# Kernel tuning notes

Hardware: AMD Instinct MI355X
Metric: run time of the kernel (lower is better)

The kernel has to match this reference:

```python
import jax, jax.numpy as jnp
import numpy as np

B, C, H, W = 8, 256, 64, 64
IC = 64  # inter_channels


def conv1x1(x, w, b):
    # x: [B,C,H,W], w: [O,C], b: [O]
    return jnp.einsum('bchw,oc->bohw', x, w) + b[None, :, None, None]


def maxpool2(x):
    # 2x2 max pool, stride 2. x: [B,C,H,W]
    b, c, h, w = x.shape
    return x.reshape(b, c, h // 2, 2, w // 2, 2).max(axis=(3, 5))


def setup_inputs() -> dict:
    key = jax.random.key(0)
    ks = jax.random.split(key, 9)
    s_in = 1.0 / np.sqrt(C)
    s_ic = 1.0 / np.sqrt(IC)
    return {
        'x': jax.random.normal(ks[0], (B, C, H, W), dtype=jnp.float32),
        'g_w': jax.random.uniform(ks[1], (IC, C), jnp.float32, -s_in, s_in),
        'g_b': jax.random.uniform(ks[2], (IC,), jnp.float32, -s_in, s_in),
        'theta_w': jax.random.uniform(ks[3], (IC, C), jnp.float32, -s_in, s_in),
        'theta_b': jax.random.uniform(ks[4], (IC,), jnp.float32, -s_in, s_in),
        'phi_w': jax.random.uniform(ks[5], (IC, C), jnp.float32, -s_in, s_in),
        'phi_b': jax.random.uniform(ks[6], (IC,), jnp.float32, -s_in, s_in),
        'W_w': jax.random.uniform(ks[7], (C, IC), jnp.float32, -np.sqrt(6.0 / IC), np.sqrt(6.0 / IC)),
        'W_b': jax.random.uniform(ks[8], (C,), jnp.float32, -s_ic, s_ic),
    }


def reference(x, g_w, g_b, theta_w, theta_b, phi_w, phi_b, W_w, W_b):
    b, c, h, w = x.shape
    n = h * w                     # query positions
    m = (h // 2) * (w // 2)       # pooled key/value positions

    v = maxpool2(conv1x1(x, g_w, g_b)).reshape(b, IC, m).transpose(0, 2, 1)   # [b,m,ic]
    q = conv1x1(x, theta_w, theta_b).reshape(b, IC, n).transpose(0, 2, 1)     # [b,n,ic]
    k = maxpool2(conv1x1(x, phi_w, phi_b)).reshape(b, IC, m)                  # [b,ic,m]

    attn = jax.nn.softmax(jnp.einsum('bni,bim->bnm', q, k), axis=-1)          # [b,n,m]
    attended = jnp.einsum('bnm,bmi->bni', attn, v)                            # [b,n,ic]
    attended = attended.transpose(0, 2, 1).reshape(b, IC, h, w)
    # F.interpolate to (h,w) is identity here: attended already has spatial (h,w)
    return conv1x1(attended, W_w, W_b) + x
```

## Files before the change

kernel.cpp:

```cpp
#include <hip/hip_runtime.h>

typedef unsigned short ushort_t;
typedef unsigned int   uint_t;

typedef __attribute__((ext_vector_type(8))) short  short8;
typedef __attribute__((ext_vector_type(4))) short  short4v;
typedef __attribute__((ext_vector_type(4))) float  float4v;

#define BB    8
#define CC    256
#define HH    64
#define WW2   64
#define NPIX  4096
#define MPOS  1024
#define ICH   64

__device__ __forceinline__ float bf2f(ushort_t u) {
  return __uint_as_float(((uint_t)u) << 16);
}
__device__ __forceinline__ ushort_t f2bf(float f) {
  uint_t i = __float_as_uint(f);
  uint_t r = (i + 0x7FFFu + ((i >> 16) & 1u)) >> 16;
  return (ushort_t)r;
}
__device__ __forceinline__ ushort_t f2bf_rna(float f) {
  return (ushort_t)((__float_as_uint(f) + 0x8000u) >> 16);
}
__device__ __forceinline__ uint_t pack2(float a, float b) {
  return (uint_t)f2bf(a) | ((uint_t)f2bf(b) << 16);
}

__global__ __launch_bounds__(256) void prep_kernel(
    const float* __restrict__ theta_w, const float* __restrict__ phi_w,
    const float* __restrict__ g_w, const float* __restrict__ W_w,
    const float* __restrict__ theta_b, const float* __restrict__ phi_b,
    const float* __restrict__ g_b,
    ushort_t* __restrict__ wA2, ushort_t* __restrict__ Wbf2,
    float* __restrict__ biasAll) {
  int i = blockIdx.x * 256 + threadIdx.x;
  if (i < 49152) {
    float v = (i < 16384) ? theta_w[i]
            : (i < 32768) ? phi_w[i - 16384]
                          : g_w[i - 32768];
    int o = i >> 8, c = i & 255;
    wA2[(c >> 3) * 1536 + o * 8 + (c & 7)] = f2bf(v);
  } else if (i < 65536) {
    int j = i - 49152;
    int o = j >> 6, ic = j & 63;
    Wbf2[(ic >> 3) * 2048 + o * 8 + (ic & 7)] = f2bf(W_w[j]);
  } else if (i < 65600)    biasAll[i - 65536] = theta_b[i - 65536];
  else if (i < 65664)      biasAll[i - 65536] = phi_b[i - 65600];
  else if (i < 65728)      biasAll[i - 65536] = g_b[i - 65664];
}

__global__ __launch_bounds__(256, 2) void qkv_kernel(
    const float* __restrict__ x, const ushort_t* __restrict__ wA2,
    const float* __restrict__ biasAll,
    ushort_t* __restrict__ qbuf, ushort_t* __restrict__ kTbuf,
    ushort_t* __restrict__ vTbuf) {
  __shared__ __align__(16) ushort_t Bsu[64 * 256];
  uint4* Bs16 = (uint4*)Bsu;
  int tid = threadIdx.x;
  int wave = tid >> 6, lane = tid & 63;
  int quad = lane >> 4, col = lane & 15;
  int b = blockIdx.x >> 6, t = blockIdx.x & 63;
  int rj = t >> 1, h = t & 1;

  {
    int pos = tid & 63, cg = tid >> 6;
    int prow = pos >> 5, pcol = pos & 31;
    const float* xsrc = x + (size_t)b * (CC * NPIX) +
                        (size_t)(2 * rj + prow) * WW2 + h * 32 + pcol;
#pragma unroll
    for (int g = 0; g < 8; ++g) {
      float v[8];
#pragma unroll
      for (int j = 0; j < 8; ++j)
        v[j] = xsrc[(size_t)(cg * 64 + g * 8 + j) * NPIX];
      uint4 w;
      w.x = pack2(v[0], v[1]);
      w.y = pack2(v[2], v[3]);
      w.z = pack2(v[4], v[5]);
      w.w = pack2(v[6], v[7]);
      int jb = cg * 8 + g;
      Bs16[pos * 32 + (jb & ~7) + ((jb & 7) ^ (pos & 7))] = w;
    }
  }
  __syncthreads();

  float4v acc[3][4];
#pragma unroll
  for (int ot = 0; ot < 3; ++ot) {
    int ob = wave * 48 + ot * 16 + quad * 4;
    float4v bv;
#pragma unroll
    for (int r = 0; r < 4; ++r) bv[r] = biasAll[ob + r];
#pragma unroll
    for (int s = 0; s < 4; ++s) acc[ot][s] = bv;
  }

  const uint4* wA16 = (const uint4*)wA2;
#pragma unroll
  for (int ks = 0; ks < 8; ++ks) {
    int kblk = ks * 4 + quad;
    short8 aw[3];
#pragma unroll
    for (int ot = 0; ot < 3; ++ot) {
      uint4 a = wA16[kblk * 192 + wave * 48 + ot * 16 + col];
      aw[ot] = *(const short8*)&a;
    }
#pragma unroll
    for (int s = 0; s < 4; ++s) {
      int lp = s * 16 + col;
      uint4 braw = Bs16[lp * 32 + (kblk & ~7) + ((kblk & 7) ^ (lp & 7))];
      short8 bx = *(const short8*)&braw;
#pragma unroll
      for (int ot = 0; ot < 3; ++ot)
        acc[ot][s] = __builtin_amdgcn_mfma_f32_16x16x32_bf16(aw[ot], bx, acc[ot][s], 0, 0, 0);
    }
  }

#pragma unroll
  for (int ot = 0; ot < 3; ++ot) {
    int ob = wave * 48 + ot * 16;
    if (ob < 64) {
#pragma unroll
      for (int s = 0; s < 4; ++s) {
        int n = (2 * rj + (s >> 1)) * WW2 + h * 32 + (s & 1) * 16 + col;
        uint2 u;
        u.x = pack2(acc[ot][s][0], acc[ot][s][1]);
        u.y = pack2(acc[ot][s][2], acc[ot][s][3]);
        *(uint2*)&qbuf[((size_t)(b * NPIX + n)) * ICH + ob + quad * 4] = u;
      }
    } else if (ob < 128) {
#pragma unroll
      for (int s = 0; s < 2; ++s) {
        float4v pm;
#pragma unroll
        for (int r = 0; r < 4; ++r) {
          float v = fmaxf(acc[ot][s][r], acc[ot][s + 2][r]);
          pm[r] = fmaxf(v, __shfl_xor(v, 1));
        }
        if ((lane & 1) == 0) {
          int m = rj * 32 + h * 16 + s * 8 + (col >> 1);
          uint2 u;
          u.x = pack2(pm[0], pm[1]);
          u.y = pack2(pm[2], pm[3]);
          *(uint2*)&kTbuf[((size_t)(b * MPOS + m)) * ICH + (ob - 64) + quad * 4] = u;
        }
      }
    } else {
#pragma unroll
      for (int s = 0; s < 2; ++s) {
        float4v pm;
#pragma unroll
        for (int r = 0; r < 4; ++r) {
          float v = fmaxf(acc[ot][s][r], acc[ot][s + 2][r]);
          pm[r] = fmaxf(v, __shfl_xor(v, 1));
        }
        if ((lane & 1) == 0) {
          int m = rj * 32 + h * 16 + s * 8 + (col >> 1);
#pragma unroll
          for (int r = 0; r < 4; ++r)
            vTbuf[((size_t)(b * ICH + (ob - 128) + quad * 4 + r)) * MPOS + m] = f2bf(pm[r]);
        }
      }
    }
  }
}

__global__ __launch_bounds__(256, 2) void attn_out_kernel(
    const ushort_t* __restrict__ qbuf, const ushort_t* __restrict__ kTbuf,
    const ushort_t* __restrict__ vTbuf, const ushort_t* __restrict__ Wbf2,
    const float* __restrict__ W_b, const float* __restrict__ x,
    float* __restrict__ out) {
  __shared__ __align__(16) ushort_t Ks[2][64 * 64];
  __shared__ __align__(16) ushort_t Vs[2][64 * 64];
  __shared__ __align__(16) ushort_t Ps[64 * 72];
  int tid  = threadIdx.x;
  int wave = tid >> 6, lane = tid & 63;
  int quad = lane >> 4, col = lane & 15;
  int b = blockIdx.x >> 6, qt = blockIdx.x & 63;

  const ushort_t* qrow = qbuf + ((size_t)(b * NPIX + qt * 64 + wave * 16 + col)) * ICH;
  short8 aQ0 = *(const short8*)&qrow[quad * 8];
  short8 aQ1 = *(const short8*)&qrow[32 + quad * 8];

  int krow0 = tid >> 3,           kblk0 = tid & 7;
  int krow1 = (tid + 256) >> 3,   kblk1 = tid & 7;
  int vic = tid >> 2, vseg = tid & 3;

  const uint4* ksrc0 = (const uint4*)(kTbuf + ((size_t)(b * MPOS)) * ICH);
  const ushort_t* vbase = vTbuf + ((size_t)(b * ICH + vic)) * MPOS;

  {
    uint4 k0 = ksrc0[tid], k1 = ksrc0[tid + 256];
    const uint4* vsrc = (const uint4*)(vbase + vseg * 16);
    uint4 v0 = vsrc[0], v1 = vsrc[1];
    *(uint4*)&Ks[0][krow0 * 64 + ((kblk0 ^ (krow0 & 7)) * 8)] = k0;
    *(uint4*)&Ks[0][krow1 * 64 + ((kblk1 ^ (krow1 & 7)) * 8)] = k1;
    *(uint4*)&Vs[0][vic * 64 + (((vseg * 2 + 0) ^ (vic & 7)) * 8)] = v0;
    *(uint4*)&Vs[0][vic * 64 + (((vseg * 2 + 1) ^ (vic & 7)) * 8)] = v1;
  }
  __syncthreads();

  const float4v zero4 = {0.f, 0.f, 0.f, 0.f};
  float l_lane[4] = {0.f, 0.f, 0.f, 0.f};
  float4v o_acc[4];
#pragma unroll
  for (int t = 0; t < 4; ++t) o_acc[t] = zero4;

  for (int kt = 0; kt < 16; ++kt) {
    uint4 nk0, nk1, nv0, nv1;
    if (kt < 15) {
      const uint4* ksrc = (const uint4*)(kTbuf + ((size_t)(b * MPOS + (kt + 1) * 64)) * ICH);
      nk0 = ksrc[tid];
      nk1 = ksrc[tid + 256];
      const uint4* vsrc = (const uint4*)(vbase + (kt + 1) * 64 + vseg * 16);
      nv0 = vsrc[0];
      nv1 = vsrc[1];
    }
    int buf = kt & 1;

    float4v s_acc[4];
#pragma unroll
    for (int t = 0; t < 4; ++t) {
      float4v s = zero4;
      short8 bk0 = *(const short8*)&Ks[buf][(t * 16 + col) * 64 + ((quad ^ (col & 7)) * 8)];
      s = __builtin_amdgcn_mfma_f32_16x16x32_bf16(aQ0, bk0, s, 0, 0, 0);
      short8 bk1 = *(const short8*)&Ks[buf][(t * 16 + col) * 64 + (((4 + quad) ^ (col & 7)) * 8)];
      s = __builtin_amdgcn_mfma_f32_16x16x32_bf16(aQ1, bk1, s, 0, 0, 0);
      s_acc[t] = s;
    }

#pragma unroll
    for (int r = 0; r < 4; ++r) {
      int prow = (wave * 16 + quad * 4 + r) * 72;
#pragma unroll
      for (int t = 0; t < 4; ++t) {
        float pv = __expf(s_acc[t][r]);
        l_lane[r] += pv;
        Ps[prow + t * 16 + col] = f2bf_rna(pv);
      }
    }

#pragma unroll
    for (int kk = 0; kk < 2; ++kk) {
      short8 ap = *(const short8*)&Ps[(wave * 16 + col) * 72 + kk * 32 + quad * 8];
#pragma unroll
      for (int t = 0; t < 4; ++t) {
        short8 bv = *(const short8*)&Vs[buf][(t * 16 + col) * 64 + (((kk * 4 + quad) ^ (col & 7)) * 8)];
        o_acc[t] = __builtin_amdgcn_mfma_f32_16x16x32_bf16(ap, bv, o_acc[t], 0, 0, 0);
      }
    }

    if (kt < 15) {
      int nbuf = buf ^ 1;
      *(uint4*)&Ks[nbuf][krow0 * 64 + ((kblk0 ^ (krow0 & 7)) * 8)] = nk0;
      *(uint4*)&Ks[nbuf][krow1 * 64 + ((kblk1 ^ (krow1 & 7)) * 8)] = nk1;
      *(uint4*)&Vs[nbuf][vic * 64 + (((vseg * 2 + 0) ^ (vic & 7)) * 8)] = nv0;
      *(uint4*)&Vs[nbuf][vic * 64 + (((vseg * 2 + 1) ^ (vic & 7)) * 8)] = nv1;
      __syncthreads();
    }
  }

#pragma unroll
  for (int r = 0; r < 4; ++r) {
    float l = l_lane[r];
    l += __shfl_xor(l, 1);
    l += __shfl_xor(l, 2);
    l += __shfl_xor(l, 4);
    l += __shfl_xor(l, 8);
    float inv = 1.0f / l;
    int prow = (wave * 16 + quad * 4 + r) * 72;
#pragma unroll
    for (int t = 0; t < 4; ++t)
      Ps[prow + t * 16 + col] = f2bf(o_acc[t][r] * inv);
  }

  float4v cacc[16];
#pragma unroll
  for (int ot = 0; ot < 16; ++ot) {
    float bv = W_b[ot * 16 + col];
    float4v bvec = {bv, bv, bv, bv};
    cacc[ot] = bvec;
  }
  const uint4* W16 = (const uint4*)Wbf2;
#pragma unroll
  for (int ks = 0; ks < 2; ++ks) {
    short8 ap = *(const short8*)&Ps[(wave * 16 + col) * 72 + ks * 32 + quad * 8];
#pragma unroll
    for (int ot = 0; ot < 16; ++ot) {
      uint4 wr = W16[(ks * 4 + quad) * 256 + ot * 16 + col];
      short8 wf = *(const short8*)&wr;
      cacc[ot] = __builtin_amdgcn_mfma_f32_16x16x32_bf16(ap, wf, cacc[ot], 0, 0, 0);
    }
  }

  int pbase = qt * 64 + wave * 16 + quad * 4;
#pragma unroll
  for (int ot = 0; ot < 16; ++ot) {
    int o = ot * 16 + col;
    size_t idx = ((size_t)(b * CC + o)) * NPIX + pbase;
    float4 xv = *(const float4*)&x[idx];
    float4 ov;
    ov.x = cacc[ot][0] + xv.x;
    ov.y = cacc[ot][1] + xv.y;
    ov.z = cacc[ot][2] + xv.z;
    ov.w = cacc[ot][3] + xv.w;
    *(float4*)&out[idx] = ov;
  }
}

extern "C" void kernel_launch(void* const* d_in, const int* in_sizes, int n_in,
                              void* d_out, int out_size, void* d_ws, size_t ws_size,
                              hipStream_t stream) {
  const float* x       = (const float*)d_in[0];
  const float* g_w     = (const float*)d_in[1];
  const float* g_b     = (const float*)d_in[2];
  const float* theta_w = (const float*)d_in[3];
  const float* theta_b = (const float*)d_in[4];
  const float* phi_w   = (const float*)d_in[5];
  const float* phi_b   = (const float*)d_in[6];
  const float* W_w     = (const float*)d_in[7];
  const float* W_b     = (const float*)d_in[8];
  (void)in_sizes; (void)n_in; (void)out_size; (void)ws_size;

  char* ws = (char*)d_ws;
  ushort_t* wA2     = (ushort_t*)(ws + 0);
  ushort_t* Wbf2    = (ushort_t*)(ws + 98304);
  float*    biasAll = (float*)(ws + 131072);
  ushort_t* qbuf    = (ushort_t*)(ws + 262144);
  ushort_t* kTbuf   = (ushort_t*)(ws + 4456448);
  ushort_t* vTbuf   = (ushort_t*)(ws + 5505024);
  float* out = (float*)d_out;

  prep_kernel<<<257, 256, 0, stream>>>(theta_w, phi_w, g_w, W_w,
                                       theta_b, phi_b, g_b,
                                       wA2, Wbf2, biasAll);
  qkv_kernel<<<512, 256, 0, stream>>>(x, wA2, biasAll, qbuf, kTbuf, vTbuf);
  attn_out_kernel<<<512, 256, 0, stream>>>(qbuf, kTbuf, vTbuf, Wbf2, W_b, x, out);
}
```

Baseline: 132.2 us.

## Split key range across wave halves in attention and halve qkv tile

The attention kernel now uses 512 threads. Two groups of four waves each take half of the key/value tiles for the same 64 queries. Their softmax denominators are combined through shared memory, and each half then computes half of the output channels from both partial P@V results. The x residual load is hoisted before the output GEMM, and s_setprio is raised around the MFMA sections. The qkv kernel uses smaller 32-position tiles over twice as many blocks with higher occupancy bounds. The goal is more parallelism and latency hiding, at the cost of losing K/V double buffering and adding extra barriers.

```diff
diff --git a/kernel.cpp b/kernel.cpp
--- a/kernel.cpp
+++ b/kernel.cpp
@@ -53,50 +53,50 @@
   else if (i < 65728)      biasAll[i - 65536] = g_b[i - 65664];
 }
 
-__global__ __launch_bounds__(256, 2) void qkv_kernel(
+__global__ __launch_bounds__(256, 4) void qkv_kernel(
     const float* __restrict__ x, const ushort_t* __restrict__ wA2,
     const float* __restrict__ biasAll,
     ushort_t* __restrict__ qbuf, ushort_t* __restrict__ kTbuf,
     ushort_t* __restrict__ vTbuf) {
-  __shared__ __align__(16) ushort_t Bsu[64 * 256];
+  __shared__ __align__(16) ushort_t Bsu[32 * 256];
   uint4* Bs16 = (uint4*)Bsu;
   int tid = threadIdx.x;
   int wave = tid >> 6, lane = tid & 63;
   int quad = lane >> 4, col = lane & 15;
-  int b = blockIdx.x >> 6, t = blockIdx.x & 63;
-  int rj = t >> 1, h = t & 1;
+  int b = blockIdx.x >> 7, t = blockIdx.x & 127;
+  int rj = t >> 2, cq = t & 3;
 
   {
-    int pos = tid & 63, cg = tid >> 6;
-    int prow = pos >> 5, pcol = pos & 31;
+    int pos = tid & 31, cg = tid >> 5;
+    int prow = pos >> 4, pcol = pos & 15;
     const float* xsrc = x + (size_t)b * (CC * NPIX) +
-                        (size_t)(2 * rj + prow) * WW2 + h * 32 + pcol;
-#pragma unroll
-    for (int g = 0; g < 8; ++g) {
+                        (size_t)(2 * rj + prow) * WW2 + cq * 16 + pcol;
+#pragma unroll
+    for (int g = 0; g < 4; ++g) {
       float v[8];
 #pragma unroll
       for (int j = 0; j < 8; ++j)
-        v[j] = xsrc[(size_t)(cg * 64 + g * 8 + j) * NPIX];
+        v[j] = xsrc[(size_t)(cg * 32 + g * 8 + j) * NPIX];
       uint4 w;
       w.x = pack2(v[0], v[1]);
       w.y = pack2(v[2], v[3]);
       w.z = pack2(v[4], v[5]);
       w.w = pack2(v[6], v[7]);
-      int jb = cg * 8 + g;
+      int jb = cg * 4 + g;
       Bs16[pos * 32 + (jb & ~7) + ((jb & 7) ^ (pos & 7))] = w;
     }
   }
   __syncthreads();
 
-  float4v acc[3][4];
+  float4v acc[3][2];
 #pragma unroll
   for (int ot = 0; ot < 3; ++ot) {
     int ob = wave * 48 + ot * 16 + quad * 4;
     float4v bv;
 #pragma unroll
     for (int r = 0; r < 4; ++r) bv[r] = biasAll[ob + r];
-#pragma unroll
-    for (int s = 0; s < 4; ++s) acc[ot][s] = bv;
+    acc[ot][0] = bv;
+    acc[ot][1] = bv;
   }
 
   const uint4* wA16 = (const uint4*)wA2;
@@ -110,7 +110,7 @@
       aw[ot] = *(const short8*)&a;
     }
 #pragma unroll
-    for (int s = 0; s < 4; ++s) {
+    for (int s = 0; s < 2; ++s) {
       int lp = s * 16 + col;
       uint4 braw = Bs16[lp * 32 + (kblk & ~7) + ((kblk & 7) ^ (lp & 7))];
       short8 bx = *(const short8*)&braw;
@@ -125,82 +125,81 @@
     int ob = wave * 48 + ot * 16;
     if (ob < 64) {
 #pragma unroll
-      for (int s = 0; s < 4; ++s) {
-        int n = (2 * rj + (s >> 1)) * WW2 + h * 32 + (s & 1) * 16 + col;
+      for (int s = 0; s < 2; ++s) {
+        int n = (2 * rj + s) * WW2 + cq * 16 + col;
         uint2 u;
         u.x = pack2(acc[ot][s][0], acc[ot][s][1]);
         u.y = pack2(acc[ot][s][2], acc[ot][s][3]);
         *(uint2*)&qbuf[((size_t)(b * NPIX + n)) * ICH + ob + quad * 4] = u;
       }
     } else if (ob < 128) {
-#pragma unroll
-      for (int s = 0; s < 2; ++s) {
-        float4v pm;
-#pragma unroll
-        for (int r = 0; r < 4; ++r) {
-          float v = fmaxf(acc[ot][s][r], acc[ot][s + 2][r]);
-          pm[r] = fmaxf(v, __shfl_xor(v, 1));
-        }
-        if ((lane & 1) == 0) {
-          int m = rj * 32 + h * 16 + s * 8 + (col >> 1);
-          uint2 u;
-          u.x = pack2(pm[0], pm[1]);
-          u.y = pack2(pm[2], pm[3]);
-          *(uint2*)&kTbuf[((size_t)(b * MPOS + m)) * ICH + (ob - 64) + quad * 4] = u;
-        }
+      float4v pm;
+#pragma unroll
+      for (int r = 0; r < 4; ++r) {
+        float v = fmaxf(acc[ot][0][r], acc[ot][1][r]);
+        pm[r] = fmaxf(v, __shfl_xor(v, 1));
+      }
+      if ((lane & 1) == 0) {
+        int m = rj * 32 + cq * 8 + (col >> 1);
+        uint2 u;
+        u.x = pack2(pm[0], pm[1]);
+        u.y = pack2(pm[2], pm[3]);
+        *(uint2*)&kTbuf[((size_t)(b * MPOS + m)) * ICH + (ob - 64) + quad * 4] = u;
       }
     } else {
-#pragma unroll
-      for (int s = 0; s < 2; ++s) {
-        float4v pm;
-#pragma unroll
-        for (int r = 0; r < 4; ++r) {
-          float v = fmaxf(acc[ot][s][r], acc[ot][s + 2][r]);
-          pm[r] = fmaxf(v, __shfl_xor(v, 1));
-        }
-        if ((lane & 1) == 0) {
-          int m = rj * 32 + h * 16 + s * 8 + (col >> 1);
-#pragma unroll
-          for (int r = 0; r < 4; ++r)
-            vTbuf[((size_t)(b * ICH + (ob - 128) + quad * 4 + r)) * MPOS + m] = f2bf(pm[r]);
-        }
-      }
-    }
-  }
-}
-
-__global__ __launch_bounds__(256, 2) void attn_out_kernel(
+      float4v pm;
+#pragma unroll
+      for (int r = 0; r < 4; ++r) {
+        float v = fmaxf(acc[ot][0][r], acc[ot][1][r]);
+        pm[r] = fmaxf(v, __shfl_xor(v, 1));
+      }
+      if ((lane & 1) == 0) {
+        int m = rj * 32 + cq * 8 + (col >> 1);
+#pragma unroll
+        for (int r = 0; r < 4; ++r)
+          vTbuf[((size_t)(b * ICH + (ob - 128) + quad * 4 + r)) * MPOS + m] = f2bf(pm[r]);
+      }
+    }
+  }
+}
+
+__global__ __launch_bounds__(512, 2) void attn_out_kernel(
     const ushort_t* __restrict__ qbuf, const ushort_t* __restrict__ kTbuf,
     const ushort_t* __restrict__ vTbuf, const ushort_t* __restrict__ Wbf2,
     const float* __restrict__ W_b, const float* __restrict__ x,
     float* __restrict__ out) {
-  __shared__ __align__(16) ushort_t Ks[2][64 * 64];
-  __shared__ __align__(16) ushort_t Vs[2][64 * 64];
-  __shared__ __align__(16) ushort_t Ps[64 * 72];
+  __shared__ __align__(16) ushort_t SH[25600];
   int tid  = threadIdx.x;
-  int wave = tid >> 6, lane = tid & 63;
+  int wid  = tid >> 6, lane = tid & 63;
   int quad = lane >> 4, col = lane & 15;
+  int wrow = wid & 3, whalf = wid >> 2;
   int b = blockIdx.x >> 6, qt = blockIdx.x & 63;
-
-  const ushort_t* qrow = qbuf + ((size_t)(b * NPIX + qt * 64 + wave * 16 + col)) * ICH;
+  int hid = tid & 255;
+
+  ushort_t* Ksh = SH + whalf * 4096;
+  ushort_t* Vsh = SH + 8192 + whalf * 4096;
+  ushort_t* Psh = SH + 16384 + whalf * 4608;
+
+  const ushort_t* qrow = qbuf + ((size_t)(b * NPIX + qt * 64 + wrow * 16 + col)) * ICH;
   short8 aQ0 = *(const short8*)&qrow[quad * 8];
   short8 aQ1 = *(const short8*)&qrow[32 + quad * 8];
 
-  int krow0 = tid >> 3,           kblk0 = tid & 7;
-  int krow1 = (tid + 256) >> 3,   kblk1 = tid & 7;
-  int vic = tid >> 2, vseg = tid & 3;
-
-  const uint4* ksrc0 = (const uint4*)(kTbuf + ((size_t)(b * MPOS)) * ICH);
+  int krow0 = hid >> 3,         kblk0 = hid & 7;
+  int krow1 = (hid + 256) >> 3, kblk1 = hid & 7;
+  int vic = hid >> 2, vseg = hid & 3;
+  int ktbase = whalf * 8;
+
+  const uint4* ksrc = (const uint4*)(kTbuf + (size_t)b * MPOS * ICH);
   const ushort_t* vbase = vTbuf + ((size_t)(b * ICH + vic)) * MPOS;
 
   {
-    uint4 k0 = ksrc0[tid], k1 = ksrc0[tid + 256];
-    const uint4* vsrc = (const uint4*)(vbase + vseg * 16);
+    uint4 k0 = ksrc[ktbase * 512 + hid], k1 = ksrc[ktbase * 512 + 256 + hid];
+    const uint4* vsrc = (const uint4*)(vbase + ktbase * 64 + vseg * 16);
     uint4 v0 = vsrc[0], v1 = vsrc[1];
-    *(uint4*)&Ks[0][krow0 * 64 + ((kblk0 ^ (krow0 & 7)) * 8)] = k0;
-    *(uint4*)&Ks[0][krow1 * 64 + ((kblk1 ^ (krow1 & 7)) * 8)] = k1;
-    *(uint4*)&Vs[0][vic * 64 + (((vseg * 2 + 0) ^ (vic & 7)) * 8)] = v0;
-    *(uint4*)&Vs[0][vic * 64 + (((vseg * 2 + 1) ^ (vic & 7)) * 8)] = v1;
+    *(uint4*)&Ksh[krow0 * 64 + ((kblk0 ^ (krow0 & 7)) * 8)] = k0;
+    *(uint4*)&Ksh[krow1 * 64 + ((kblk1 ^ (krow1 & 7)) * 8)] = k1;
+    *(uint4*)&Vsh[vic * 64 + (((vseg * 2 + 0) ^ (vic & 7)) * 8)] = v0;
+    *(uint4*)&Vsh[vic * 64 + (((vseg * 2 + 1) ^ (vic & 7)) * 8)] = v1;
   }
   __syncthreads();
 
@@ -210,104 +209,130 @@
 #pragma unroll
   for (int t = 0; t < 4; ++t) o_acc[t] = zero4;
 
-  for (int kt = 0; kt < 16; ++kt) {
+  for (int i = 0; i < 8; ++i) {
     uint4 nk0, nk1, nv0, nv1;
-    if (kt < 15) {
-      const uint4* ksrc = (const uint4*)(kTbuf + ((size_t)(b * MPOS + (kt + 1) * 64)) * ICH);
-      nk0 = ksrc[tid];
-      nk1 = ksrc[tid + 256];
-      const uint4* vsrc = (const uint4*)(vbase + (kt + 1) * 64 + vseg * 16);
+    if (i < 7) {
+      int kt = ktbase + i + 1;
+      nk0 = ksrc[kt * 512 + hid];
+      nk1 = ksrc[kt * 512 + 256 + hid];
+      const uint4* vsrc = (const uint4*)(vbase + kt * 64 + vseg * 16);
       nv0 = vsrc[0];
       nv1 = vsrc[1];
     }
-    int buf = kt & 1;
 
     float4v s_acc[4];
+    __builtin_amdgcn_s_setprio(1);
 #pragma unroll
     for (int t = 0; t < 4; ++t) {
       float4v s = zero4;
-      short8 bk0 = *(const short8*)&Ks[buf][(t * 16 + col) * 64 + ((quad ^ (col & 7)) * 8)];
+      short8 bk0 = *(const short8*)&Ksh[(t * 16 + col) * 64 + ((quad ^ (col & 7)) * 8)];
       s = __builtin_amdgcn_mfma_f32_16x16x32_bf16(aQ0, bk0, s, 0, 0, 0);
-      short8 bk1 = *(const short8*)&Ks[buf][(t * 16 + col) * 64 + (((4 + quad) ^ (col & 7)) * 8)];
+      short8 bk1 = *(const short8*)&Ksh[(t * 16 + col) * 64 + (((4 + quad) ^ (col & 7)) * 8)];
       s = __builtin_amdgcn_mfma_f32_16x16x32_bf16(aQ1, bk1, s, 0, 0, 0);
       s_acc[t] = s;
     }
+    __builtin_amdgcn_s_setprio(0);
 
 #pragma unroll
     for (int r = 0; r < 4; ++r) {
-      int prow = (wave * 16 + quad * 4 + r) * 72;
+      int prow = (wrow * 16 + quad * 4 + r) * 72;
 #pragma unroll
       for (int t = 0; t < 4; ++t) {
         float pv = __expf(s_acc[t][r]);
         l_lane[r] += pv;
-        Ps[prow + t * 16 + col] = f2bf_rna(pv);
-      }
-    }
-
+        Psh[prow + t * 16 + col] = f2bf_rna(pv);
+      }
+    }
+
+    __builtin_amdgcn_s_setprio(1);
 #pragma unroll
     for (int kk = 0; kk < 2; ++kk) {
-      short8 ap = *(const short8*)&Ps[(wave * 16 + col) * 72 + kk * 32 + quad * 8];
+      short8 ap = *(const short8*)&Psh[(wrow * 16 + col) * 72 + kk * 32 + quad * 8];
 #pragma unroll
       for (int t = 0; t < 4; ++t) {
-        short8 bv = *(const short8*)&Vs[buf][(t * 16 + col) * 64 + (((kk * 4 + quad) ^ (col & 7)) * 8)];
+        short8 bv = *(const short8*)&Vsh[(t * 16 + col) * 64 + (((kk * 4 + quad) ^ (col & 7)) * 8)];
         o_acc[t] = __builtin_amdgcn_mfma_f32_16x16x32_bf16(ap, bv, o_acc[t], 0, 0, 0);
       }
     }
-
-    if (kt < 15) {
-      int nbuf = buf ^ 1;
-      *(uint4*)&Ks[nbuf][krow0 * 64 + ((kblk0 ^ (krow0 & 7)) * 8)] = nk0;
-      *(uint4*)&Ks[nbuf][krow1 * 64 + ((kblk1 ^ (krow1 & 7)) * 8)] = nk1;
-      *(uint4*)&Vs[nbuf][vic * 64 + (((vseg * 2 + 0) ^ (vic & 7)) * 8)] = nv0;
-      *(uint4*)&Vs[nbuf][vic * 64 + (((vseg * 2 + 1) ^ (vic & 7)) * 8)] = nv1;
-      __syncthreads();
-    }
-  }
-
+    __builtin_amdgcn_s_setprio(0);
+
+    __syncthreads();
+    if (i < 7) {
+      *(uint4*)&Ksh[krow0 * 64 + ((kblk0 ^ (krow0 & 7)) * 8)] = nk0;
+      *(uint4*)&Ksh[krow1 * 64 + ((kblk1 ^ (krow1 & 7)) * 8)] = nk1;
+      *(uint4*)&Vsh[vic * 64 + (((vseg * 2 + 0) ^ (vic & 7)) * 8)] = nv0;
+      *(uint4*)&Vsh[vic * 64 + (((vseg * 2 + 1) ^ (vic & 7)) * 8)] = nv1;
+    }
+    __syncthreads();
+  }
+
+  float* lbuf = (float*)SH;
+#pragma unroll
+  for (int r = 0; r < 4; ++r) lbuf[tid * 4 + r] = l_lane[r];
+  __syncthreads();
+  float inv_l[4];
 #pragma unroll
   for (int r = 0; r < 4; ++r) {
-    float l = l_lane[r];
+    float l = l_lane[r] + lbuf[(tid ^ 256) * 4 + r];
     l += __shfl_xor(l, 1);
     l += __shfl_xor(l, 2);
     l += __shfl_xor(l, 4);
     l += __shfl_xor(l, 8);
-    float inv = 1.0f / l;
-    int prow = (wave * 16 + quad * 4 + r) * 72;
+    inv_l[r] = 1.0f / l;
+  }
+
+#pragma unroll
+  for (int r = 0; r < 4; ++r) {
+    int prow = (wrow * 16 + quad * 4 + r) * 72;
 #pragma unroll
     for (int t = 0; t < 4; ++t)
-      Ps[prow + t * 16 + col] = f2bf(o_acc[t][r] * inv);
-  }
-
-  float4v cacc[16];
-#pragma unroll
-  for (int ot = 0; ot < 16; ++ot) {
-    float bv = W_b[ot * 16 + col];
+      Psh[prow + t * 16 + col] = f2bf(o_acc[t][r] * inv_l[r]);
+  }
+  __syncthreads();
+
+  float4v cacc[8];
+#pragma unroll
+  for (int ot = 0; ot < 8; ++ot) {
+    float bv = W_b[whalf * 128 + ot * 16 + col];
     float4v bvec = {bv, bv, bv, bv};
     cacc[ot] = bvec;
   }
+
+  int pbase = qt * 64 + wrow * 16 + quad * 4;
+  float4 xv[8];
+#pragma unroll
+  for (int ot = 0; ot < 8; ++ot) {
+    int o = whalf * 128 + ot * 16 + col;
+    xv[ot] = *(const float4*)&x[((size_t)(b * CC + o)) * NPIX + pbase];
+  }
+
   const uint4* W16 = (const uint4*)Wbf2;
-#pragma unroll
-  for (int ks = 0; ks < 2; ++ks) {
-    short8 ap = *(const short8*)&Ps[(wave * 16 + col) * 72 + ks * 32 + quad * 8];
-#pragma unroll
-    for (int ot = 0; ot < 16; ++ot) {
-      uint4 wr = W16[(ks * 4 + quad) * 256 + ot * 16 + col];
-      short8 wf = *(const short8*)&wr;
-      cacc[ot] = __builtin_amdgcn_mfma_f32_16x16x32_bf16(ap, wf, cacc[ot], 0, 0, 0);
-    }
-  }
-
-  int pbase = qt * 64 + wave * 16 + quad * 4;
-#pragma unroll
-  for (int ot = 0; ot < 16; ++ot) {
-    int o = ot * 16 + col;
+  __builtin_amdgcn_s_setprio(1);
+#pragma unroll
+  for (int h = 0; h < 2; ++h) {
+    const ushort_t* Ph = SH + 16384 + h * 4608;
+#pragma unroll
+    for (int ks = 0; ks < 2; ++ks) {
+      short8 ap = *(const short8*)&Ph[(wrow * 16 + col) * 72 + ks * 32 + quad * 8];
+#pragma unroll
+      for (int ot = 0; ot < 8; ++ot) {
+        uint4 wr = W16[(ks * 4 + quad) * 256 + whalf * 128 + ot * 16 + col];
+        short8 wf = *(const short8*)&wr;
+        cacc[ot] = __builtin_amdgcn_mfma_f32_16x16x32_bf16(ap, wf, cacc[ot], 0, 0, 0);
+      }
+    }
+  }
+  __builtin_amdgcn_s_setprio(0);
+
+#pragma unroll
+  for (int ot = 0; ot < 8; ++ot) {
+    int o = whalf * 128 + ot * 16 + col;
     size_t idx = ((size_t)(b * CC + o)) * NPIX + pbase;
-    float4 xv = *(const float4*)&x[idx];
     float4 ov;
-    ov.x = cacc[ot][0] + xv.x;
-    ov.y = cacc[ot][1] + xv.y;
-    ov.z = cacc[ot][2] + xv.z;
-    ov.w = cacc[ot][3] + xv.w;
+    ov.x = cacc[ot][0] + xv[ot].x;
+    ov.y = cacc[ot][1] + xv[ot].y;
+    ov.z = cacc[ot][2] + xv[ot].z;
+    ov.w = cacc[ot][3] + xv[ot].w;
     *(float4*)&out[idx] = ov;
   }
 }
@@ -338,6 +363,6 @@
   prep_kernel<<<257, 256, 0, stream>>>(theta_w, phi_w, g_w, W_w,
                                        theta_b, phi_b, g_b,
                                        wA2, Wbf2, biasAll);
-  qkv_kernel<<<512, 256, 0, stream>>>(x, wA2, biasAll, qbuf, kTbuf, vTbuf);
-  attn_out_kernel<<<512, 256, 0, stream>>>(qbuf, kTbuf, vTbuf, Wbf2, W_b, x, out);
-}
+  qkv_kernel<<<1024, 256, 0, stream>>>(x, wA2, biasAll, qbuf, kTbuf, vTbuf);
+  attn_out_kernel<<<512, 512, 0, stream>>>(qbuf, kTbuf, vTbuf, Wbf2, W_b, x, out);
+}
```

Measured after the change: 137.5 us. +4.0%, slower.

## Load K/V fragments directly from global into registers per wave, drop LDS staging

Applied to the files above, without the earlier changes.

The attention kernel now gives each wave its own independent 16-query job and reads K and V MFMA operands straight from global memory (L2/L1) into registers. K is double-buffered in registers across steps, and LDS is kept only for a per-wave P tile. This removes the block-wide __syncthreads and the LDS store/load traffic for K/V, and adds s_setprio hints around the MFMA sections. The output projection is restructured to compute each output tile and store it immediately, which lowers register pressure. In exchange, each wave reloads the whole K/V for its batch from cache, raising global/L2 traffic fourfold versus block-shared staging. The launch grid must also match the new job mapping in the unseen launcher.

```diff
diff --git a/kernel.cpp b/kernel.cpp
--- a/kernel.cpp
+++ b/kernel.cpp
@@ -174,35 +174,25 @@
     const ushort_t* __restrict__ vTbuf, const ushort_t* __restrict__ Wbf2,
     const float* __restrict__ W_b, const float* __restrict__ x,
     float* __restrict__ out) {
-  __shared__ __align__(16) ushort_t Ks[2][64 * 64];
-  __shared__ __align__(16) ushort_t Vs[2][64 * 64];
-  __shared__ __align__(16) ushort_t Ps[64 * 72];
+  __shared__ __align__(16) ushort_t Ps[4][16 * 72];
   int tid  = threadIdx.x;
-  int wave = tid >> 6, lane = tid & 63;
+  int wid  = tid >> 6, lane = tid & 63;
   int quad = lane >> 4, col = lane & 15;
-  int b = blockIdx.x >> 6, qt = blockIdx.x & 63;
-
-  const ushort_t* qrow = qbuf + ((size_t)(b * NPIX + qt * 64 + wave * 16 + col)) * ICH;
+  int job  = blockIdx.x * 4 + wid;
+  int b    = job >> 8;
+  int qbase = (job & 255) * 16;
+
+  ushort_t* Psw = &Ps[wid][0];
+
+  const ushort_t* kb = kTbuf + (size_t)b * MPOS * ICH;
+  const ushort_t* vb = vTbuf + (size_t)b * ICH * MPOS;
+
+  const ushort_t* qrow = qbuf + ((size_t)(b * NPIX + qbase + col)) * ICH;
   short8 aQ0 = *(const short8*)&qrow[quad * 8];
   short8 aQ1 = *(const short8*)&qrow[32 + quad * 8];
 
-  int krow0 = tid >> 3,           kblk0 = tid & 7;
-  int krow1 = (tid + 256) >> 3,   kblk1 = tid & 7;
-  int vic = tid >> 2, vseg = tid & 3;
-
-  const uint4* ksrc0 = (const uint4*)(kTbuf + ((size_t)(b * MPOS)) * ICH);
-  const ushort_t* vbase = vTbuf + ((size_t)(b * ICH + vic)) * MPOS;
-
-  {
-    uint4 k0 = ksrc0[tid], k1 = ksrc0[tid + 256];
-    const uint4* vsrc = (const uint4*)(vbase + vseg * 16);
-    uint4 v0 = vsrc[0], v1 = vsrc[1];
-    *(uint4*)&Ks[0][krow0 * 64 + ((kblk0 ^ (krow0 & 7)) * 8)] = k0;
-    *(uint4*)&Ks[0][krow1 * 64 + ((kblk1 ^ (krow1 & 7)) * 8)] = k1;
-    *(uint4*)&Vs[0][vic * 64 + (((vseg * 2 + 0) ^ (vic & 7)) * 8)] = v0;
-    *(uint4*)&Vs[0][vic * 64 + (((vseg * 2 + 1) ^ (vic & 7)) * 8)] = v1;
-  }
-  __syncthreads();
+  const ushort_t* kbase = kb + col * ICH + quad * 8;
+  const ushort_t* vbase = vb + (size_t)col * MPOS + quad * 8;
 
   const float4v zero4 = {0.f, 0.f, 0.f, 0.f};
   float l_lane[4] = {0.f, 0.f, 0.f, 0.f};
@@ -210,59 +200,65 @@
 #pragma unroll
   for (int t = 0; t < 4; ++t) o_acc[t] = zero4;
 
-  for (int kt = 0; kt < 16; ++kt) {
-    uint4 nk0, nk1, nv0, nv1;
-    if (kt < 15) {
-      const uint4* ksrc = (const uint4*)(kTbuf + ((size_t)(b * MPOS + (kt + 1) * 64)) * ICH);
-      nk0 = ksrc[tid];
-      nk1 = ksrc[tid + 256];
-      const uint4* vsrc = (const uint4*)(vbase + (kt + 1) * 64 + vseg * 16);
-      nv0 = vsrc[0];
-      nv1 = vsrc[1];
-    }
-    int buf = kt & 1;
-
-    float4v s_acc[4];
-#pragma unroll
-    for (int t = 0; t < 4; ++t) {
-      float4v s = zero4;
-      short8 bk0 = *(const short8*)&Ks[buf][(t * 16 + col) * 64 + ((quad ^ (col & 7)) * 8)];
-      s = __builtin_amdgcn_mfma_f32_16x16x32_bf16(aQ0, bk0, s, 0, 0, 0);
-      short8 bk1 = *(const short8*)&Ks[buf][(t * 16 + col) * 64 + (((4 + quad) ^ (col & 7)) * 8)];
-      s = __builtin_amdgcn_mfma_f32_16x16x32_bf16(aQ1, bk1, s, 0, 0, 0);
-      s_acc[t] = s;
-    }
-
-#pragma unroll
-    for (int r = 0; r < 4; ++r) {
-      int prow = (wave * 16 + quad * 4 + r) * 72;
-#pragma unroll
-      for (int t = 0; t < 4; ++t) {
-        float pv = __expf(s_acc[t][r]);
-        l_lane[r] += pv;
-        Ps[prow + t * 16 + col] = f2bf_rna(pv);
-      }
-    }
-
-#pragma unroll
-    for (int kk = 0; kk < 2; ++kk) {
-      short8 ap = *(const short8*)&Ps[(wave * 16 + col) * 72 + kk * 32 + quad * 8];
-#pragma unroll
-      for (int t = 0; t < 4; ++t) {
-        short8 bv = *(const short8*)&Vs[buf][(t * 16 + col) * 64 + (((kk * 4 + quad) ^ (col & 7)) * 8)];
-        o_acc[t] = __builtin_amdgcn_mfma_f32_16x16x32_bf16(ap, bv, o_acc[t], 0, 0, 0);
-      }
-    }
-
-    if (kt < 15) {
-      int nbuf = buf ^ 1;
-      *(uint4*)&Ks[nbuf][krow0 * 64 + ((kblk0 ^ (krow0 & 7)) * 8)] = nk0;
-      *(uint4*)&Ks[nbuf][krow1 * 64 + ((kblk1 ^ (krow1 & 7)) * 8)] = nk1;
-      *(uint4*)&Vs[nbuf][vic * 64 + (((vseg * 2 + 0) ^ (vic & 7)) * 8)] = nv0;
-      *(uint4*)&Vs[nbuf][vic * 64 + (((vseg * 2 + 1) ^ (vic & 7)) * 8)] = nv1;
-      __syncthreads();
-    }
-  }
+  short8 kfA[8], kfB[8];
+
+#define LOADK(dst, kt)                                                        \
+  _Pragma("unroll")                                                           \
+  for (int t = 0; t < 4; ++t) {                                               \
+    dst[t * 2 + 0] = *(const short8*)&kbase[((kt) * 64 + t * 16) * 64];       \
+    dst[t * 2 + 1] = *(const short8*)&kbase[((kt) * 64 + t * 16) * 64 + 32];  \
+  }
+
+  LOADK(kfA, 0);
+
+#define STEP(kcur, knext, kt)                                                 \
+  {                                                                           \
+    short8 vf[8];                                                             \
+    _Pragma("unroll")                                                         \
+    for (int t = 0; t < 4; ++t) {                                             \
+      _Pragma("unroll")                                                       \
+      for (int kk = 0; kk < 2; ++kk)                                          \
+        vf[t * 2 + kk] =                                                      \
+            *(const short8*)&vbase[t * 16 * MPOS + (kt) * 64 + kk * 32];      \
+    }                                                                         \
+    if ((kt) < 15) { LOADK(knext, (kt) + 1); }                                \
+    float4v s_acc[4];                                                         \
+    __builtin_amdgcn_s_setprio(1);                                            \
+    _Pragma("unroll")                                                         \
+    for (int t = 0; t < 4; ++t) {                                             \
+      float4v s = zero4;                                                      \
+      s = __builtin_amdgcn_mfma_f32_16x16x32_bf16(aQ0, kcur[t * 2 + 0], s, 0, 0, 0); \
+      s = __builtin_amdgcn_mfma_f32_16x16x32_bf16(aQ1, kcur[t * 2 + 1], s, 0, 0, 0); \
+      s_acc[t] = s;                                                           \
+    }                                                                         \
+    __builtin_amdgcn_s_setprio(0);                                            \
+    _Pragma("unroll")                                                         \
+    for (int r = 0; r < 4; ++r) {                                             \
+      int prow = (quad * 4 + r) * 72;                                         \
+      _Pragma("unroll")                                                       \
+      for (int t = 0; t < 4; ++t) {                                           \
+        float pv = __expf(s_acc[t][r]);                                       \
+        l_lane[r] += pv;                                                      \
+        Psw[prow + t * 16 + col] = f2bf_rna(pv);                              \
+      }                                                                       \
+    }                                                                         \
+    __builtin_amdgcn_s_setprio(1);                                            \
+    _Pragma("unroll")                                                         \
+    for (int kk = 0; kk < 2; ++kk) {                                          \
+      short8 ap = *(const short8*)&Psw[col * 72 + kk * 32 + quad * 8];        \
+      _Pragma("unroll")                                                       \
+      for (int t = 0; t < 4; ++t)                                             \
+        o_acc[t] = __builtin_amdgcn_mfma_f32_16x16x32_bf16(ap, vf[t * 2 + kk], o_acc[t], 0, 0, 0); \
+    }                                                                         \
+    __builtin_amdgcn_s_setprio(0);                                            \
+  }
+
+  for (int i = 0; i < 8; ++i) {
+    STEP(kfA, kfB, 2 * i);
+    STEP(kfB, kfA, 2 * i + 1);
+  }
+#undef STEP
+#undef LOADK
 
 #pragma unroll
   for (int r = 0; r < 4; ++r) {
@@ -272,42 +268,31 @@
     l += __shfl_xor(l, 4);
     l += __shfl_xor(l, 8);
     float inv = 1.0f / l;
-    int prow = (wave * 16 + quad * 4 + r) * 72;
+    int prow = (quad * 4 + r) * 72;
 #pragma unroll
     for (int t = 0; t < 4; ++t)
-      Ps[prow + t * 16 + col] = f2bf(o_acc[t][r] * inv);
-  }
-
-  float4v cacc[16];
+      Psw[prow + t * 16 + col] = f2bf(o_acc[t][r] * inv);
+  }
+
+  short8 ap0 = *(const short8*)&Psw[col * 72 + quad * 8];
+  short8 ap1 = *(const short8*)&Psw[col * 72 + 32 + quad * 8];
+  const uint4* W16 = (const uint4*)Wbf2;
+  int pbase = qbase + quad * 4;
 #pragma unroll
   for (int ot = 0; ot < 16; ++ot) {
-    float bv = W_b[ot * 16 + col];
-    float4v bvec = {bv, bv, bv, bv};
-    cacc[ot] = bvec;
-  }
-  const uint4* W16 = (const uint4*)Wbf2;
-#pragma unroll
-  for (int ks = 0; ks < 2; ++ks) {
-    short8 ap = *(const short8*)&Ps[(wave * 16 + col) * 72 + ks * 32 + quad * 8];
-#pragma unroll
-    for (int ot = 0; ot < 16; ++ot) {
-      uint4 wr = W16[(ks * 4 + quad) * 256 + ot * 16 + col];
-      short8 wf = *(const short8*)&wr;
-      cacc[ot] = __builtin_amdgcn_mfma_f32_16x16x32_bf16(ap, wf, cacc[ot], 0, 0, 0);
-    }
-  }
-
-  int pbase = qt * 64 + wave * 16 + quad * 4;
-#pragma unroll
-  for (int ot = 0; ot < 16; ++ot) {
-    int o = ot * 16 + col;
-    size_t idx = ((size_t)(b * CC + o)) * NPIX + pbase;
+    float bvv = W_b[ot * 16 + col];
+    float4v c = {bvv, bvv, bvv, bvv};
+    uint4 w0 = W16[quad * 256 + ot * 16 + col];
+    uint4 w1 = W16[(4 + quad) * 256 + ot * 16 + col];
+    c = __builtin_amdgcn_mfma_f32_16x16x32_bf16(ap0, *(const short8*)&w0, c, 0, 0, 0);
+    c = __builtin_amdgcn_mfma_f32_16x16x32_bf16(ap1, *(const short8*)&w1, c, 0, 0, 0);
+    size_t idx = ((size_t)(b * CC + ot * 16 + col)) * NPIX + pbase;
     float4 xv = *(const float4*)&x[idx];
     float4 ov;
-    ov.x = cacc[ot][0] + xv.x;
-    ov.y = cacc[ot][1] + xv.y;
-    ov.z = cacc[ot][2] + xv.z;
-    ov.w = cacc[ot][3] + xv.w;
+    ov.x = c[0] + xv.x;
+    ov.y = c[1] + xv.y;
+    ov.z = c[2] + xv.z;
+    ov.w = c[3] + xv.w;
     *(float4*)&out[idx] = ov;
   }
 }
```

Result: slower. 167.5 us (+26.7%).

## Stage K/V via direct global-to-LDS loads, transpose S tile, per-wave P buffers

Applied to the files above, without the earlier changes.

The attention kernel now loads K and V tiles straight from global memory into LDS with global_load_lds, so the register round-trip and the separate LDS stores are gone. The score MFMA swaps its operands, which lets each lane hold four consecutive keys and write P with packed 8-byte stores into a per-wave buffer. It also adds s_setprio around the MFMA phases and fuses the output projection with the residual store so fewer accumulator registers stay live. The risks are correctness of the swizzled direct-to-LDS addressing and a __syncthreads that now runs on every iteration.

```diff
diff --git a/kernel.cpp b/kernel.cpp
--- a/kernel.cpp
+++ b/kernel.cpp
@@ -28,6 +28,12 @@
 }
 __device__ __forceinline__ uint_t pack2(float a, float b) {
   return (uint_t)f2bf(a) | ((uint_t)f2bf(b) << 16);
+}
+
+__device__ __forceinline__ void gl2lds16(const ushort_t* g, ushort_t* l) {
+  __builtin_amdgcn_global_load_lds(
+      (const __attribute__((address_space(1))) void*)g,
+      (__attribute__((address_space(3))) void*)l, 16, 0, 0);
 }
 
 __global__ __launch_bounds__(256) void prep_kernel(
@@ -176,138 +182,122 @@
     float* __restrict__ out) {
   __shared__ __align__(16) ushort_t Ks[2][64 * 64];
   __shared__ __align__(16) ushort_t Vs[2][64 * 64];
-  __shared__ __align__(16) ushort_t Ps[64 * 72];
+  __shared__ __align__(16) ushort_t Ps[4][16 * 72];
   int tid  = threadIdx.x;
   int wave = tid >> 6, lane = tid & 63;
   int quad = lane >> 4, col = lane & 15;
   int b = blockIdx.x >> 6, qt = blockIdx.x & 63;
 
+  ushort_t* Psw = &Ps[wave][0];
+
   const ushort_t* qrow = qbuf + ((size_t)(b * NPIX + qt * 64 + wave * 16 + col)) * ICH;
   short8 aQ0 = *(const short8*)&qrow[quad * 8];
   short8 aQ1 = *(const short8*)&qrow[32 + quad * 8];
 
-  int krow0 = tid >> 3,           kblk0 = tid & 7;
-  int krow1 = (tid + 256) >> 3,   kblk1 = tid & 7;
-  int vic = tid >> 2, vseg = tid & 3;
-
-  const uint4* ksrc0 = (const uint4*)(kTbuf + ((size_t)(b * MPOS)) * ICH);
-  const ushort_t* vbase = vTbuf + ((size_t)(b * ICH + vic)) * MPOS;
-
-  {
-    uint4 k0 = ksrc0[tid], k1 = ksrc0[tid + 256];
-    const uint4* vsrc = (const uint4*)(vbase + vseg * 16);
-    uint4 v0 = vsrc[0], v1 = vsrc[1];
-    *(uint4*)&Ks[0][krow0 * 64 + ((kblk0 ^ (krow0 & 7)) * 8)] = k0;
-    *(uint4*)&Ks[0][krow1 * 64 + ((kblk1 ^ (krow1 & 7)) * 8)] = k1;
-    *(uint4*)&Vs[0][vic * 64 + (((vseg * 2 + 0) ^ (vic & 7)) * 8)] = v0;
-    *(uint4*)&Vs[0][vic * 64 + (((vseg * 2 + 1) ^ (vic & 7)) * 8)] = v1;
-  }
+  int srow = tid >> 3, sblk = tid & 7;
+  int swz  = (sblk ^ (srow & 7)) * 8;
+  const ushort_t* kg = kTbuf + (size_t)b * MPOS * ICH;
+  const ushort_t* vg = vTbuf + (size_t)b * ICH * MPOS;
+  const ushort_t* kg0 = kg + srow * ICH + swz;
+  const ushort_t* kg1 = kg + (32 + srow) * ICH + swz;
+  const ushort_t* vg0 = vg + (size_t)srow * MPOS + swz;
+  const ushort_t* vg1 = vg + (size_t)(32 + srow) * MPOS + swz;
+
+#define STAGE(bufi, kt)                                          \
+  do {                                                           \
+    gl2lds16(kg0 + (kt) * 4096, &Ks[bufi][wave * 512]);          \
+    gl2lds16(kg1 + (kt) * 4096, &Ks[bufi][2048 + wave * 512]);   \
+    gl2lds16(vg0 + (kt) * 64,   &Vs[bufi][wave * 512]);          \
+    gl2lds16(vg1 + (kt) * 64,   &Vs[bufi][2048 + wave * 512]);   \
+  } while (0)
+
+  STAGE(0, 0);
   __syncthreads();
 
   const float4v zero4 = {0.f, 0.f, 0.f, 0.f};
-  float l_lane[4] = {0.f, 0.f, 0.f, 0.f};
+  float l_lane = 0.f;
   float4v o_acc[4];
 #pragma unroll
   for (int t = 0; t < 4; ++t) o_acc[t] = zero4;
 
   for (int kt = 0; kt < 16; ++kt) {
-    uint4 nk0, nk1, nv0, nv1;
-    if (kt < 15) {
-      const uint4* ksrc = (const uint4*)(kTbuf + ((size_t)(b * MPOS + (kt + 1) * 64)) * ICH);
-      nk0 = ksrc[tid];
-      nk1 = ksrc[tid + 256];
-      const uint4* vsrc = (const uint4*)(vbase + (kt + 1) * 64 + vseg * 16);
-      nv0 = vsrc[0];
-      nv1 = vsrc[1];
-    }
     int buf = kt & 1;
+    if (kt < 15) STAGE(buf ^ 1, kt + 1);
 
     float4v s_acc[4];
+    __builtin_amdgcn_s_setprio(1);
 #pragma unroll
     for (int t = 0; t < 4; ++t) {
       float4v s = zero4;
-      short8 bk0 = *(const short8*)&Ks[buf][(t * 16 + col) * 64 + ((quad ^ (col & 7)) * 8)];
-      s = __builtin_amdgcn_mfma_f32_16x16x32_bf16(aQ0, bk0, s, 0, 0, 0);
-      short8 bk1 = *(const short8*)&Ks[buf][(t * 16 + col) * 64 + (((4 + quad) ^ (col & 7)) * 8)];
-      s = __builtin_amdgcn_mfma_f32_16x16x32_bf16(aQ1, bk1, s, 0, 0, 0);
+      short8 ak0 = *(const short8*)&Ks[buf][(t * 16 + col) * 64 + ((quad ^ (col & 7)) * 8)];
+      s = __builtin_amdgcn_mfma_f32_16x16x32_bf16(ak0, aQ0, s, 0, 0, 0);
+      short8 ak1 = *(const short8*)&Ks[buf][(t * 16 + col) * 64 + (((4 + quad) ^ (col & 7)) * 8)];
+      s = __builtin_amdgcn_mfma_f32_16x16x32_bf16(ak1, aQ1, s, 0, 0, 0);
       s_acc[t] = s;
     }
-
-#pragma unroll
-    for (int r = 0; r < 4; ++r) {
-      int prow = (wave * 16 + quad * 4 + r) * 72;
-#pragma unroll
-      for (int t = 0; t < 4; ++t) {
-        float pv = __expf(s_acc[t][r]);
-        l_lane[r] += pv;
-        Ps[prow + t * 16 + col] = f2bf_rna(pv);
-      }
-    }
-
+    __builtin_amdgcn_s_setprio(0);
+
+#pragma unroll
+    for (int t = 0; t < 4; ++t) {
+      float p0 = __expf(s_acc[t][0]);
+      float p1 = __expf(s_acc[t][1]);
+      float p2 = __expf(s_acc[t][2]);
+      float p3 = __expf(s_acc[t][3]);
+      l_lane += (p0 + p1) + (p2 + p3);
+      uint2 u;
+      u.x = (uint_t)f2bf_rna(p0) | ((uint_t)f2bf_rna(p1) << 16);
+      u.y = (uint_t)f2bf_rna(p2) | ((uint_t)f2bf_rna(p3) << 16);
+      *(uint2*)&Psw[col * 72 + t * 16 + quad * 4] = u;
+    }
+
+    __builtin_amdgcn_s_setprio(1);
 #pragma unroll
     for (int kk = 0; kk < 2; ++kk) {
-      short8 ap = *(const short8*)&Ps[(wave * 16 + col) * 72 + kk * 32 + quad * 8];
+      short8 ap = *(const short8*)&Psw[col * 72 + kk * 32 + quad * 8];
 #pragma unroll
       for (int t = 0; t < 4; ++t) {
         short8 bv = *(const short8*)&Vs[buf][(t * 16 + col) * 64 + (((kk * 4 + quad) ^ (col & 7)) * 8)];
         o_acc[t] = __builtin_amdgcn_mfma_f32_16x16x32_bf16(ap, bv, o_acc[t], 0, 0, 0);
       }
     }
-
-    if (kt < 15) {
-      int nbuf = buf ^ 1;
-      *(uint4*)&Ks[nbuf][krow0 * 64 + ((kblk0 ^ (krow0 & 7)) * 8)] = nk0;
-      *(uint4*)&Ks[nbuf][krow1 * 64 + ((kblk1 ^ (krow1 & 7)) * 8)] = nk1;
-      *(uint4*)&Vs[nbuf][vic * 64 + (((vseg * 2 + 0) ^ (vic & 7)) * 8)] = nv0;
-      *(uint4*)&Vs[nbuf][vic * 64 + (((vseg * 2 + 1) ^ (vic & 7)) * 8)] = nv1;
-      __syncthreads();
-    }
-  }
+    __builtin_amdgcn_s_setprio(0);
+
+    __syncthreads();
+  }
+#undef STAGE
+
+  l_lane += __shfl_xor(l_lane, 16);
+  l_lane += __shfl_xor(l_lane, 32);
+  float invl = 1.0f / l_lane;
 
 #pragma unroll
   for (int r = 0; r < 4; ++r) {
-    float l = l_lane[r];
-    l += __shfl_xor(l, 1);
-    l += __shfl_xor(l, 2);
-    l += __shfl_xor(l, 4);
-    l += __shfl_xor(l, 8);
-    float inv = 1.0f / l;
-    int prow = (wave * 16 + quad * 4 + r) * 72;
+    float iv = __shfl(invl, (lane & 48) | (quad * 4 + r));
+    int prow = (quad * 4 + r) * 72;
 #pragma unroll
     for (int t = 0; t < 4; ++t)
-      Ps[prow + t * 16 + col] = f2bf(o_acc[t][r] * inv);
-  }
-
-  float4v cacc[16];
+      Psw[prow + t * 16 + col] = f2bf(o_acc[t][r] * iv);
+  }
+
+  short8 ap0 = *(const short8*)&Psw[col * 72 + quad * 8];
+  short8 ap1 = *(const short8*)&Psw[col * 72 + 32 + quad * 8];
+  const uint4* W16 = (const uint4*)Wbf2;
+  int pbase = qt * 64 + wave * 16 + quad * 4;
 #pragma unroll
   for (int ot = 0; ot < 16; ++ot) {
-    float bv = W_b[ot * 16 + col];
-    float4v bvec = {bv, bv, bv, bv};
-    cacc[ot] = bvec;
-  }
-  const uint4* W16 = (const uint4*)Wbf2;
-#pragma unroll
-  for (int ks = 0; ks < 2; ++ks) {
-    short8 ap = *(const short8*)&Ps[(wave * 16 + col) * 72 + ks * 32 + quad * 8];
-#pragma unroll
-    for (int ot = 0; ot < 16; ++ot) {
-      uint4 wr = W16[(ks * 4 + quad) * 256 + ot * 16 + col];
-      short8 wf = *(const short8*)&wr;
-      cacc[ot] = __builtin_amdgcn_mfma_f32_16x16x32_bf16(ap, wf, cacc[ot], 0, 0, 0);
-    }
-  }
-
-  int pbase = qt * 64 + wave * 16 + quad * 4;
-#pragma unroll
-  for (int ot = 0; ot < 16; ++ot) {
-    int o = ot * 16 + col;
-    size_t idx = ((size_t)(b * CC + o)) * NPIX + pbase;
+    float bvv = W_b[ot * 16 + col];
+    float4v c = {bvv, bvv, bvv, bvv};
+    uint4 w0 = W16[quad * 256 + ot * 16 + col];
+    uint4 w1 = W16[(4 + quad) * 256 + ot * 16 + col];
+    c = __builtin_amdgcn_mfma_f32_16x16x32_bf16(ap0, *(const short8*)&w0, c, 0, 0, 0);
+    c = __builtin_amdgcn_mfma_f32_16x16x32_bf16(ap1, *(const short8*)&w1, c, 0, 0, 0);
+    size_t idx = ((size_t)(b * CC + ot * 16 + col)) * NPIX + pbase;
     float4 xv = *(const float4*)&x[idx];
     float4 ov;
-    ov.x = cacc[ot][0] + xv.x;
-    ov.y = cacc[ot][1] + xv.y;
-    ov.z = cacc[ot][2] + xv.z;
-    ov.w = cacc[ot][3] + xv.w;
+    ov.x = c[0] + xv.x;
+    ov.y = c[1] + xv.y;
+    ov.z = c[2] + xv.z;
+    ov.w = c[3] + xv.w;
     *(float4*)&out[idx] = ov;
   }
 }
```

After: 131.1 us. About the same (-0.8%).
